# Kernel optimization log

Measured on AMD Instinct MI355X. Metric: run time of the kernel, lower is better.

The kernel has to match this reference:

```python
import jax, jax.numpy as jnp
import numpy as np

B, L, D_MODEL, N_HEADS = 4, 2048, 1024, 16
HEAD_DIM = D_MODEL // N_HEADS


def setup_inputs() -> dict:
    key = jax.random.key(0)
    ks = jax.random.split(key, 11)
    s = 1.0 / np.sqrt(D_MODEL)
    return {
        "queries": jax.random.normal(ks[0], (B, L, D_MODEL), jnp.float32),
        "keys": jax.random.normal(ks[1], (B, L, D_MODEL), jnp.float32),
        "values": jax.random.normal(ks[2], (B, L, D_MODEL), jnp.float32),
        "Wq": jax.random.normal(ks[3], (D_MODEL, D_MODEL), jnp.float32) * s,
        "bq": jnp.zeros((D_MODEL,), jnp.float32),
        "Wk": jax.random.normal(ks[4], (D_MODEL, D_MODEL), jnp.float32) * s,
        "bk": jnp.zeros((D_MODEL,), jnp.float32),
        "Wv": jax.random.normal(ks[5], (D_MODEL, D_MODEL), jnp.float32) * s,
        "bv": jnp.zeros((D_MODEL,), jnp.float32),
        "Wo": jax.random.normal(ks[6], (D_MODEL, D_MODEL), jnp.float32) * s,
        "bo": jnp.zeros((D_MODEL,), jnp.float32),
    }


def reference(queries, keys, values, Wq, bq, Wk, bk, Wv, bv, Wo, bo):
    Bsz, Lq, _ = queries.shape
    S = keys.shape[1]
    H, E = N_HEADS, HEAD_DIM
    # QKV projections (weights stored [in, out])
    q = (queries @ Wq + bq).reshape(Bsz, Lq, H, E)
    k = (keys @ Wk + bk).reshape(Bsz, S, H, E)
    v = (values @ Wv + bv).reshape(Bsz, S, H, E)
    scale = 1.0 / np.sqrt(E)
    # scores: [B, H, L, S]
    scores = jnp.einsum("blhe,bshe->bhls", q, k)
    A = jax.nn.softmax(scale * scores, axis=-1)
    # context: [B, L, H, E] -> [B, L, D]
    ctx = jnp.einsum("bhls,bshd->blhd", A, v).reshape(Bsz, Lq, H * E)
    out = ctx @ Wo + bo
    return out
```

## Files before the change

### kernel.cpp

```cpp
#include <hip/hip_runtime.h>

#define BATCH 4
#define SEQ   2048
#define DMODEL 1024
#define NHEADS 16
#define HDIM  64
#define MROWS (BATCH * SEQ)

typedef float f32x4 __attribute__((ext_vector_type(4)));
typedef short s16x8 __attribute__((ext_vector_type(8)));
typedef short s16x4 __attribute__((ext_vector_type(4)));
typedef unsigned short u16;

#define MFMA32K(a, b, c) __builtin_amdgcn_mfma_f32_16x16x32_bf16((a), (b), (c), 0, 0, 0)
#define MFMA16K(a, b, c) __builtin_amdgcn_mfma_f32_16x16x16bf16_1k((a), (b), (c), 0, 0, 0)

__device__ __forceinline__ u16 f2bf(float x) {
    unsigned int u = __builtin_bit_cast(unsigned int, x);
    unsigned int r = u + 0x7fffu + ((u >> 16) & 1u);
    return (u16)(r >> 16);
}

#if __has_builtin(__builtin_amdgcn_cvt_pk_bf16_f32)
__device__ __forceinline__ unsigned int pack2bf(float a, float b) {
    auto r = __builtin_amdgcn_cvt_pk_bf16_f32(a, b);
    return __builtin_bit_cast(unsigned int, r);
}
#else
__device__ __forceinline__ unsigned int pack2bf(float a, float b) {
    return (unsigned int)f2bf(a) | ((unsigned int)f2bf(b) << 16);
}
#endif

__device__ __forceinline__ void dma16(const u16* g, const u16* l) {
    __builtin_amdgcn_global_load_lds(
        (const __attribute__((address_space(1))) unsigned int*)g,
        (__attribute__((address_space(3))) unsigned int*)l, 16, 0, 0);
}

__global__ __launch_bounds__(256) void prep(
    const float* __restrict__ s0, const float* __restrict__ s1,
    const float* __restrict__ s2, u16* __restrict__ d0, u16* __restrict__ d1,
    u16* __restrict__ d2, const float* __restrict__ W0,
    const float* __restrict__ W1, const float* __restrict__ W2,
    const float* __restrict__ W3, u16* __restrict__ Wt) {
    __shared__ u16 tile[64][80];
    const int bid = blockIdx.x;
    const int t = threadIdx.x;
    if (bid < 12288) {
        const int z = bid >> 12, xi = bid & 4095;
        const float* src = (z == 0) ? s0 : (z == 1) ? s1 : s2;
        u16* dst = (z == 0) ? d0 : (z == 1) ? d1 : d2;
        const int i = xi * 256 + t;
        float4 a = ((const float4*)src)[i * 2];
        float4 b = ((const float4*)src)[i * 2 + 1];
        uint4 o;
        o.x = pack2bf(a.x, a.y); o.y = pack2bf(a.z, a.w);
        o.z = pack2bf(b.x, b.y); o.w = pack2bf(b.z, b.w);
        *(uint4*)(dst + (size_t)i * 8) = o;
    } else {
        const int wb = bid - 12288;
        const int mtx = wb >> 8;
        const int rem = wb & 255;
        const float* W = (mtx == 0) ? W0 : (mtx == 1) ? W1 : (mtx == 2) ? W2 : W3;
        u16* out = Wt + (size_t)mtx * DMODEL * DMODEL;
        const int n0 = (rem & 15) * 64, k0 = (rem >> 4) * 64;
#pragma unroll
        for (int j = 0; j < 4; ++j) {
            int k = j * 16 + (t >> 4);
            int c = (t & 15) * 4;
            float4 v = *(const float4*)(W + (size_t)(k0 + k) * DMODEL + n0 + c);
            tile[c + 0][k] = f2bf(v.x);
            tile[c + 1][k] = f2bf(v.y);
            tile[c + 2][k] = f2bf(v.z);
            tile[c + 3][k] = f2bf(v.w);
        }
        __syncthreads();
#pragma unroll
        for (int i2 = 0; i2 < 2; ++i2) {
            int n = i2 * 32 + (t >> 3), ck = (t & 7) * 8;
            uint4 v = *(const uint4*)(&tile[n][ck]);
            *(uint4*)(out + (size_t)(n0 + n) * DMODEL + k0 + ck) = v;
        }
    }
}

__global__ __launch_bounds__(256) void gemm_qkv(
    const u16* __restrict__ Aq, const u16* __restrict__ Ak,
    const u16* __restrict__ Av, const u16* __restrict__ Wt,
    const float* __restrict__ biq, const float* __restrict__ bik,
    const float* __restrict__ biv, u16* __restrict__ oq, u16* __restrict__ ok,
    u16* __restrict__ ov, float sq) {
    __shared__ u16 As[128 * 64];
    __shared__ u16 Bs[128 * 64];
    const int t = threadIdx.x;
    const int w = t >> 6, lane = t & 63, quad = lane >> 4, l16 = lane & 15;
    const int z = blockIdx.z;
    const u16* A = (z == 0) ? Aq : (z == 1) ? Ak : Av;
    const u16* B = Wt + (size_t)z * DMODEL * DMODEL;
    const float* bias = (z == 0) ? biq : (z == 1) ? bik : biv;
    u16* C = (z == 0) ? oq : (z == 1) ? ok : ov;
    const float scale = (z == 0) ? sq : 1.0f;
    const int m0 = blockIdx.x * 128, n0 = blockIdx.y * 128;
    const int wm = (w >> 1) * 64, wn = (w & 1) * 64;
    const int lr8 = lane >> 3;
    const int lun = (lane & 7) ^ lr8;

    f32x4 acc[4][4] = {};

    for (int k0 = 0; k0 < DMODEL; k0 += 64) {
#pragma unroll
        for (int j = 0; j < 4; ++j) {
            int r8 = w * 32 + j * 8;
            dma16(A + (size_t)(m0 + r8 + lr8) * DMODEL + k0 + lun * 8, &As[r8 * 64]);
            dma16(B + (size_t)(n0 + r8 + lr8) * DMODEL + k0 + lun * 8, &Bs[r8 * 64]);
        }
        __syncthreads();
#pragma unroll
        for (int half = 0; half < 2; ++half) {
            s16x8 af[4], bf[4];
#pragma unroll
            for (int mt = 0; mt < 4; ++mt) {
                int un = ((half * 4 + quad) ^ (l16 & 7)) * 8;
                af[mt] = *(const s16x8*)(&As[(wm + mt * 16 + l16) * 64 + un]);
                bf[mt] = *(const s16x8*)(&Bs[(wn + mt * 16 + l16) * 64 + un]);
            }
#pragma unroll
            for (int mt = 0; mt < 4; ++mt)
#pragma unroll
                for (int nt = 0; nt < 4; ++nt)
                    acc[mt][nt] = MFMA32K(af[mt], bf[nt], acc[mt][nt]);
        }
        __syncthreads();
    }

#pragma unroll
    for (int mt = 0; mt < 4; ++mt)
#pragma unroll
        for (int nt = 0; nt < 4; ++nt) {
            int col = n0 + wn + nt * 16 + l16;
            float bv_ = bias[col];
#pragma unroll
            for (int r = 0; r < 4; ++r) {
                int row = m0 + wm + mt * 16 + quad * 4 + r;
                C[(size_t)row * DMODEL + col] = f2bf((acc[mt][nt][r] + bv_) * scale);
            }
        }
}

__global__ __launch_bounds__(256) void gemm_o(const u16* __restrict__ A,
                                              const u16* __restrict__ Bt,
                                              const float* __restrict__ bias,
                                              float* __restrict__ Cp) {
    __shared__ u16 As[128 * 64];
    __shared__ u16 Bs[128 * 64];
    const int t = threadIdx.x;
    const int w = t >> 6, lane = t & 63, quad = lane >> 4, l16 = lane & 15;
    const int m0 = blockIdx.x * 128, n0 = blockIdx.y * 128;
    const int wm = (w >> 1) * 64, wn = (w & 1) * 64;
    const int lr8 = lane >> 3;
    const int lun = (lane & 7) ^ lr8;

    f32x4 acc[4][4] = {};

    for (int k0 = 0; k0 < DMODEL; k0 += 64) {
#pragma unroll
        for (int j = 0; j < 4; ++j) {
            int r8 = w * 32 + j * 8;
            dma16(A + (size_t)(m0 + r8 + lr8) * DMODEL + k0 + lun * 8, &As[r8 * 64]);
            dma16(Bt + (size_t)(n0 + r8 + lr8) * DMODEL + k0 + lun * 8, &Bs[r8 * 64]);
        }
        __syncthreads();
#pragma unroll
        for (int half = 0; half < 2; ++half) {
            s16x8 af[4], bf[4];
#pragma unroll
            for (int mt = 0; mt < 4; ++mt) {
                int un = ((half * 4 + quad) ^ (l16 & 7)) * 8;
                af[mt] = *(const s16x8*)(&As[(wm + mt * 16 + l16) * 64 + un]);
                bf[mt] = *(const s16x8*)(&Bs[(wn + mt * 16 + l16) * 64 + un]);
            }
#pragma unroll
            for (int mt = 0; mt < 4; ++mt)
#pragma unroll
                for (int nt = 0; nt < 4; ++nt)
                    acc[mt][nt] = MFMA32K(af[mt], bf[nt], acc[mt][nt]);
        }
        __syncthreads();
    }

#pragma unroll
    for (int mt = 0; mt < 4; ++mt)
#pragma unroll
        for (int nt = 0; nt < 4; ++nt) {
            int col = n0 + wn + nt * 16 + l16;
            float bv_ = bias[col];
#pragma unroll
            for (int r = 0; r < 4; ++r) {
                int row = m0 + wm + mt * 16 + quad * 4 + r;
                Cp[(size_t)row * DMODEL + col] = acc[mt][nt][r] + bv_;
            }
        }
}

__global__ __launch_bounds__(256, 2) void attn3(const u16* __restrict__ qb,
                                                const u16* __restrict__ kb,
                                                const u16* __restrict__ vb,
                                                u16* __restrict__ ctxb) {
    __shared__ u16 Ks[64 * 64];
    __shared__ u16 Vt[80 * 72];
    const int t = threadIdx.x;
    const int w = t >> 6, lane = t & 63, quad = lane >> 4, l16 = lane & 15;
    const int h = blockIdx.x, b = blockIdx.z, q0 = blockIdx.y * 256;

    s16x8 bq[4][2];
#pragma unroll
    for (int qs = 0; qs < 4; ++qs) {
        size_t base = (size_t)(b * SEQ + q0 + w * 64 + qs * 16 + l16) * DMODEL + h * HDIM + quad * 8;
        bq[qs][0] = *(const s16x8*)(qb + base);
        bq[qs][1] = *(const s16x8*)(qb + base + 32);
    }

    for (int idx = t; idx < 16 * 72; idx += 256) {
        int r = idx / 72, c = idx - r * 72;
        Vt[(64 + r) * 72 + c] = (r == 0) ? (u16)0x3F80 : (u16)0;
    }

    const int krow = lane >> 3;
    const int kunit = (lane & 7) ^ (krow & 7);

    f32x4 o[4][5] = {};

    for (int s0 = 0; s0 < SEQ; s0 += 64) {
        __syncthreads();
#pragma unroll
        for (int j = 0; j < 2; ++j) {
            int row = w * 16 + j * 8 + krow;
            dma16(kb + (size_t)(b * SEQ + s0 + row) * DMODEL + h * HDIM + kunit * 8,
                  &Ks[(w * 16 + j * 8) * 64]);
        }
#pragma unroll
        for (int i = 0; i < 2; ++i) {
            int idx = i * 256 + t;
            int key = idx >> 3, seg = idx & 7;
            union { uint4 v; u16 s[8]; } u;
            u.v = *(const uint4*)(vb + (size_t)(b * SEQ + s0 + key) * DMODEL + h * HDIM + seg * 8);
            int col = (((key >> 3) ^ seg) << 3) + (key & 7);
#pragma unroll
            for (int ii = 0; ii < 8; ++ii)
                Vt[(seg * 8 + ii) * 72 + col] = u.s[ii];
        }
        __syncthreads();

        s16x8 ak[4][2];
#pragma unroll
        for (int kt = 0; kt < 4; ++kt) {
            int row = kt * 16 + l16;
#pragma unroll
            for (int hf = 0; hf < 2; ++hf) {
                int un = (hf * 4 + quad) ^ (l16 & 7);
                ak[kt][hf] = *(const s16x8*)(&Ks[row * 64 + un * 8]);
            }
        }

        unsigned int pk[4][4][2];
#pragma unroll
        for (int qs = 0; qs < 4; ++qs) {
            f32x4 sc[4];
#pragma unroll
            for (int kt = 0; kt < 4; ++kt) {
                f32x4 zz = {0.0f, 0.0f, 0.0f, 0.0f};
                zz = MFMA32K(ak[kt][0], bq[qs][0], zz);
                sc[kt] = MFMA32K(ak[kt][1], bq[qs][1], zz);
            }
#pragma unroll
            for (int kt = 0; kt < 4; ++kt) {
                float p0 = __builtin_amdgcn_exp2f(sc[kt][0]);
                float p1 = __builtin_amdgcn_exp2f(sc[kt][1]);
                float p2 = __builtin_amdgcn_exp2f(sc[kt][2]);
                float p3 = __builtin_amdgcn_exp2f(sc[kt][3]);
                pk[qs][kt][0] = pack2bf(p0, p1);
                pk[qs][kt][1] = pack2bf(p2, p3);
            }
        }

#pragma unroll
        for (int mt = 0; mt < 5; ++mt) {
            const int dim = mt * 16 + l16;
            const int swz = (dim >> 3) & 7;
            const int rowoff = dim * 72;
#pragma unroll
            for (int kt = 0; kt < 4; ++kt) {
                int col = ((((kt * 2) + (quad >> 1)) ^ swz) << 3) + ((quad & 1) << 2);
                s16x4 av = *(const s16x4*)(&Vt[rowoff + col]);
#pragma unroll
                for (int qs = 0; qs < 4; ++qs) {
                    union { unsigned int u[2]; s16x4 v; } pb;
                    pb.u[0] = pk[qs][kt][0];
                    pb.u[1] = pk[qs][kt][1];
                    o[qs][mt] = MFMA16K(av, pb.v, o[qs][mt]);
                }
            }
        }
    }

#pragma unroll
    for (int qs = 0; qs < 4; ++qs) {
        float ls = __shfl(o[qs][4][0], l16);
        float rl = 1.0f / ls;
        size_t rowbase = (size_t)(b * SEQ + q0 + w * 64 + qs * 16 + l16) * DMODEL + h * HDIM;
#pragma unroll
        for (int mt = 0; mt < 4; ++mt)
#pragma unroll
            for (int rr = 0; rr < 2; ++rr) {
                unsigned int v = pack2bf(o[qs][mt][rr * 2] * rl, o[qs][mt][rr * 2 + 1] * rl);
                *(unsigned int*)(&ctxb[rowbase + mt * 16 + quad * 4 + rr * 2]) = v;
            }
    }
}

extern "C" void kernel_launch(void* const* d_in, const int* in_sizes, int n_in,
                              void* d_out, int out_size, void* d_ws, size_t ws_size,
                              hipStream_t stream) {
    const float* queries = (const float*)d_in[0];
    const float* keys    = (const float*)d_in[1];
    const float* values  = (const float*)d_in[2];
    const float* Wq = (const float*)d_in[3];
    const float* bq = (const float*)d_in[4];
    const float* Wk = (const float*)d_in[5];
    const float* bk = (const float*)d_in[6];
    const float* Wv = (const float*)d_in[7];
    const float* bv = (const float*)d_in[8];
    const float* Wo = (const float*)d_in[9];
    const float* bo = (const float*)d_in[10];
    float* out = (float*)d_out;

    char* ws = (char*)d_ws;
    u16* Wt   = (u16*)ws;
    u16* aq   = (u16*)(ws + ((size_t)8 << 20));
    u16* ak   = (u16*)(ws + ((size_t)24 << 20));
    u16* av   = (u16*)(ws + ((size_t)40 << 20));
    u16* qbuf = (u16*)(ws + ((size_t)56 << 20));
    u16* kbuf = (u16*)(ws + ((size_t)72 << 20));
    u16* vbuf = (u16*)(ws + ((size_t)88 << 20));
    u16* ctxb = qbuf;

    const size_t WSZ = (size_t)DMODEL * DMODEL;
    const float S2 = 0.125f * 1.44269504088896340736f;

    dim3 blk(256);

    prep<<<dim3(13312), blk, 0, stream>>>(queries, keys, values, aq, ak, av,
                                          Wq, Wk, Wv, Wo, Wt);

    gemm_qkv<<<dim3(64, 8, 3), blk, 0, stream>>>(aq, ak, av, Wt,
                                                 bq, bk, bv, qbuf, kbuf, vbuf, S2);

    attn3<<<dim3(NHEADS, SEQ / 256, BATCH), blk, 0, stream>>>(qbuf, kbuf, vbuf, ctxb);

    gemm_o<<<dim3(64, 8), blk, 0, stream>>>(ctxb, Wt + 3 * WSZ, bo, out);
}
```

Baseline: 349.4 us.

## Double-buffer QKV GEMM LDS tiles with async DMA prefetch overlap

Restructures the QKV projection GEMM main loop from a single 64-wide K tile into two ping-pong 32-wide K buffers. The next tile's global-to-LDS DMA is issued before computing the current one, and explicit vmcnt waits and raw barriers replace __syncthreads. The goal is to hide global load latency behind MFMA work. In exchange there are more iterations, each with less compute, and hand-managed waitcnt ordering that has to stay correct.

```diff
diff --git a/kernel.cpp b/kernel.cpp
--- a/kernel.cpp
+++ b/kernel.cpp
@@ -91,8 +91,10 @@
     const float* __restrict__ biq, const float* __restrict__ bik,
     const float* __restrict__ biv, u16* __restrict__ oq, u16* __restrict__ ok,
     u16* __restrict__ ov, float sq) {
-    __shared__ u16 As[128 * 64];
-    __shared__ u16 Bs[128 * 64];
+    __shared__ u16 As0[128 * 32];
+    __shared__ u16 Bs0[128 * 32];
+    __shared__ u16 As1[128 * 32];
+    __shared__ u16 Bs1[128 * 32];
     const int t = threadIdx.x;
     const int w = t >> 6, lane = t & 63, quad = lane >> 4, l16 = lane & 15;
     const int z = blockIdx.z;
@@ -103,36 +105,71 @@
     const float scale = (z == 0) ? sq : 1.0f;
     const int m0 = blockIdx.x * 128, n0 = blockIdx.y * 128;
     const int wm = (w >> 1) * 64, wn = (w & 1) * 64;
-    const int lr8 = lane >> 3;
-    const int lun = (lane & 7) ^ lr8;
+
+    const int srow = lane >> 2;
+    const int sunit = (lane & 3) ^ (srow & 3);
+    const u16* aBase = A + (size_t)(m0 + w * 32 + srow) * DMODEL + sunit * 8;
+    const u16* bBase = B + (size_t)(n0 + w * 32 + srow) * DMODEL + sunit * 8;
+    const int un8 = (quad ^ (l16 & 3)) * 8;
 
     f32x4 acc[4][4] = {};
 
-    for (int k0 = 0; k0 < DMODEL; k0 += 64) {
-#pragma unroll
-        for (int j = 0; j < 4; ++j) {
-            int r8 = w * 32 + j * 8;
-            dma16(A + (size_t)(m0 + r8 + lr8) * DMODEL + k0 + lun * 8, &As[r8 * 64]);
-            dma16(B + (size_t)(n0 + r8 + lr8) * DMODEL + k0 + lun * 8, &Bs[r8 * 64]);
-        }
-        __syncthreads();
-#pragma unroll
-        for (int half = 0; half < 2; ++half) {
-            s16x8 af[4], bf[4];
-#pragma unroll
-            for (int mt = 0; mt < 4; ++mt) {
-                int un = ((half * 4 + quad) ^ (l16 & 7)) * 8;
-                af[mt] = *(const s16x8*)(&As[(wm + mt * 16 + l16) * 64 + un]);
-                bf[mt] = *(const s16x8*)(&Bs[(wn + mt * 16 + l16) * 64 + un]);
-            }
-#pragma unroll
-            for (int mt = 0; mt < 4; ++mt)
-#pragma unroll
-                for (int nt = 0; nt < 4; ++nt)
-                    acc[mt][nt] = MFMA32K(af[mt], bf[nt], acc[mt][nt]);
-        }
-        __syncthreads();
-    }
+#define STAGE(AS_, BS_, kt_)                                                   \
+    do {                                                                       \
+        dma16(aBase + (kt_) * 32,                &AS_[(w * 32) * 32]);         \
+        dma16(aBase + 16 * DMODEL + (kt_) * 32,  &AS_[(w * 32 + 16) * 32]);    \
+        dma16(bBase + (kt_) * 32,                &BS_[(w * 32) * 32]);         \
+        dma16(bBase + 16 * DMODEL + (kt_) * 32,  &BS_[(w * 32 + 16) * 32]);    \
+    } while (0)
+
+#define WAITC4 asm volatile("s_waitcnt vmcnt(4)" ::: "memory")
+#define WAITC0 asm volatile("s_waitcnt vmcnt(0)" ::: "memory")
+#define BAR()                                                                  \
+    do {                                                                       \
+        asm volatile("s_barrier" ::: "memory");                                \
+        __builtin_amdgcn_sched_barrier(0);                                     \
+    } while (0)
+
+#define COMPUTE(AS_, BS_)                                                      \
+    do {                                                                       \
+        s16x8 af[4], bf[4];                                                    \
+        _Pragma("unroll")                                                      \
+        for (int mt = 0; mt < 4; ++mt) {                                       \
+            af[mt] = *(const s16x8*)(&AS_[(wm + mt * 16 + l16) * 32 + un8]);   \
+            bf[mt] = *(const s16x8*)(&BS_[(wn + mt * 16 + l16) * 32 + un8]);   \
+        }                                                                      \
+        _Pragma("unroll")                                                      \
+        for (int mt = 0; mt < 4; ++mt) {                                       \
+            _Pragma("unroll")                                                  \
+            for (int nt = 0; nt < 4; ++nt)                                     \
+                acc[mt][nt] = MFMA32K(af[mt], bf[nt], acc[mt][nt]);            \
+        }                                                                      \
+    } while (0)
+
+    const int NT = DMODEL / 32;
+    STAGE(As0, Bs0, 0);
+    for (int tt = 0; tt < NT - 2; tt += 2) {
+        STAGE(As1, Bs1, tt + 1);
+        WAITC4; BAR();
+        COMPUTE(As0, Bs0);
+        BAR();
+        STAGE(As0, Bs0, tt + 2);
+        WAITC4; BAR();
+        COMPUTE(As1, Bs1);
+        BAR();
+    }
+    STAGE(As1, Bs1, NT - 1);
+    WAITC4; BAR();
+    COMPUTE(As0, Bs0);
+    BAR();
+    WAITC0; BAR();
+    COMPUTE(As1, Bs1);
+
+#undef STAGE
+#undef WAITC4
+#undef WAITC0
+#undef BAR
+#undef COMPUTE
 
 #pragma unroll
     for (int mt = 0; mt < 4; ++mt)
```

Result: no change. 342.7 us (-1.9%).
